# Kernel optimization log

Hardware: AMD Instinct MI355X
Metric: run time of the kernel (lower is better)

The kernel has to match this reference:

```python
import jax, jax.numpy as jnp
import numpy as np

N, L, D, H = 2, 2048, 1024, 16
DK = D // H  # 64


def setup_inputs() -> dict:
    key = jax.random.key(0)
    ks = jax.random.split(key, 8)
    Xq = jax.random.normal(ks[0], (N, L, D), dtype=jnp.float32)
    Xk = jax.random.normal(ks[1], (N, L, D), dtype=jnp.float32)
    Xv = jax.random.normal(ks[2], (N, L, D), dtype=jnp.float32)
    mask_2d = jax.random.randint(ks[3], (N, L, L), 0, 2, dtype=jnp.int32)
    scale = 0.02
    Wq = jax.random.normal(ks[4], (D, D), dtype=jnp.float32) * scale
    Wk = jax.random.normal(ks[5], (D, D), dtype=jnp.float32) * scale
    Wv = jax.random.normal(ks[6], (D, D), dtype=jnp.float32) * scale
    Wo = jax.random.normal(ks[7], (D, D), dtype=jnp.float32) * scale
    return {"Xq": Xq, "Xk": Xk, "Xv": Xv, "Wq": Wq, "Wk": Wk, "Wv": Wv, "Wo": Wo, "mask_2d": mask_2d}


def reference(Xq, Xk, Xv, Wq, Wk, Wv, Wo, mask_2d):
    # Projections (bias=False). Per-head slicing in the original == reshape to [N,L,H,DK].
    Q = (Xq @ Wq).reshape(N, L, H, DK)
    K = (Xk @ Wk).reshape(N, L, H, DK)
    V = (Xv @ Wv).reshape(N, L, H, DK)
    # Scaled dot-product scores: [N, H, L, L]
    scores = jnp.einsum("blhd,bmhd->bhlm", Q, K) / jnp.sqrt(jnp.asarray(DK, scores_dtype(Q)))
    # NOTE: original uses masked_fill(mask==0, 0) BEFORE softmax (zero-fill, not -inf).
    scores = jnp.where(mask_2d[:, None, :, :] == 0, jnp.zeros((), scores.dtype), scores)
    A = jax.nn.softmax(scores, axis=-1)
    O = jnp.einsum("bhlm,bmhd->blhd", A, V).reshape(N, L, D)
    return O @ Wo


def scores_dtype(Q):
    return Q.dtype
```

## Files before the change

kernel.cpp:

```cpp
#include <hip/hip_runtime.h>

#define NB 2
#define L_SEQ 2048
#define NH 16
#define DKH 64
#define DMODEL 1024
#define MROWS (NB * L_SEQ)

typedef __attribute__((ext_vector_type(8))) short short8;
typedef __attribute__((ext_vector_type(4))) float f32x4;

static __device__ __forceinline__ unsigned short f2bf(float f) {
    unsigned u = __float_as_uint(f);
    u += 0x7fffu + ((u >> 16) & 1u);
    return (unsigned short)(u >> 16);
}

static __device__ __forceinline__ float fexp2(float x) {
#if __has_builtin(__builtin_amdgcn_exp2f)
    return __builtin_amdgcn_exp2f(x);
#else
    return __expf(x * 0.6931471806f);
#endif
}

static __device__ __forceinline__ void gll16(const void* g, void* l) {
    __builtin_amdgcn_global_load_lds(
        (const __attribute__((address_space(1))) void*)g,
        (__attribute__((address_space(3))) void*)l, 16, 0, 0);
}

__global__ __launch_bounds__(256)
void cast3(const float* __restrict__ s0, const float* __restrict__ s1,
           const float* __restrict__ s2, unsigned short* __restrict__ dst)
{
    const int z = blockIdx.z;
    const float* src = (z == 0) ? s0 : (z == 1) ? s1 : s2;
    const size_t i4 = (size_t)blockIdx.x * 256 + threadIdx.x;
    float4 v = ((const float4*)src)[i4];
    ushort4 o;
    o.x = f2bf(v.x); o.y = f2bf(v.y); o.z = f2bf(v.z); o.w = f2bf(v.w);
    ((ushort4*)(dst + (size_t)z * 4194304))[i4] = o;
}

__global__ __launch_bounds__(256)
void castWt(const float* __restrict__ w0, const float* __restrict__ w1,
            const float* __restrict__ w2, const float* __restrict__ w3,
            unsigned short* __restrict__ dst)
{
    __shared__ float ts[32][33];
    const int z = blockIdx.z;
    const float* W = (z == 0) ? w0 : (z == 1) ? w1 : (z == 2) ? w2 : w3;
    unsigned short* Wt = dst + (size_t)z * 1048576;

    const int k0 = blockIdx.y * 32;
    const int n0 = blockIdx.x * 32;
    const int t  = threadIdx.x;
    const int r  = t >> 3;
    const int c  = (t & 7) * 4;

    float4 v = *(const float4*)&W[(size_t)(k0 + r) * DMODEL + n0 + c];
    ts[r][c + 0] = v.x; ts[r][c + 1] = v.y; ts[r][c + 2] = v.z; ts[r][c + 3] = v.w;
    __syncthreads();

    ushort4 o;
    o.x = f2bf(ts[c + 0][r]); o.y = f2bf(ts[c + 1][r]);
    o.z = f2bf(ts[c + 2][r]); o.w = f2bf(ts[c + 3][r]);
    *(ushort4*)&Wt[(size_t)(n0 + r) * DMODEL + k0 + c] = o;
}

__global__ __launch_bounds__(256)
void maskbits(const int* __restrict__ mask, unsigned long long* __restrict__ MWT)
{
    const int lane = threadIdx.x & 63;
    const size_t wid = (size_t)blockIdx.x * 4 + (threadIdx.x >> 6);
    const int mv = mask[wid * 64 + lane];
    const unsigned long long bits = __ballot(mv != 0);
    if (lane == 0) {
        const int b   = (int)(wid >> 16);
        const int rem = (int)(wid & 65535);
        const int row = rem >> 5;
        const int wd  = rem & 31;
        MWT[((size_t)b * 32 + wd) * L_SEQ + row] = bits;
    }
}

__global__ __launch_bounds__(256)
void gemm_bf16(const unsigned short* __restrict__ Aall,
               const unsigned short* __restrict__ Ball,
               void* __restrict__ Oall,
               const int out_mode, const size_t a_zs, const size_t b_zs,
               const size_t o_zs)
{
    __shared__ __align__(16) unsigned short As[128 * 32];
    __shared__ __align__(16) unsigned short Bs[128 * 32];
    __shared__ __align__(16) unsigned short Ts[128 * 128];

    const int t    = threadIdx.x;
    const int w    = t >> 6;
    const int lane = t & 63;
    const int z    = blockIdx.z;
    const int m0   = blockIdx.y * 128;
    const int n0   = blockIdx.x * 128;

    const unsigned short* A = Aall + (size_t)z * a_zs;
    const unsigned short* B = Ball + (size_t)z * b_zs;

    const int srow = w * 32 + (lane >> 2);
    const int skc  = (lane & 3) * 8;
    const unsigned short* agp0 = A + (size_t)(m0 + srow) * DMODEL + skc;
    const unsigned short* agp1 = agp0 + (size_t)16 * DMODEL;
    const unsigned short* bgp0 = B + (size_t)(n0 + srow) * DMODEL + skc;
    const unsigned short* bgp1 = bgp0 + (size_t)16 * DMODEL;
    unsigned short* la0 = &As[w * 1024];
    unsigned short* la1 = la0 + 512;
    unsigned short* lb0 = &Bs[w * 1024];
    unsigned short* lb1 = lb0 + 512;

    const int ml = lane & 15;
    const int q  = lane >> 4;
    const int wm = (w >> 1) * 64;
    const int wn = (w & 1) * 64;

    const f32x4 z4 = {0.f, 0.f, 0.f, 0.f};
    f32x4 acc[4][4];
#pragma unroll
    for (int i = 0; i < 4; ++i)
#pragma unroll
        for (int j = 0; j < 4; ++j) acc[i][j] = z4;

    for (int kt = 0; kt < DMODEL; kt += 32) {
        __syncthreads();
        gll16(agp0 + kt, la0);
        gll16(agp1 + kt, la1);
        gll16(bgp0 + kt, lb0);
        gll16(bgp1 + kt, lb1);
        __syncthreads();

        short8 av[4], bv[4];
#pragma unroll
        for (int mt = 0; mt < 4; ++mt)
            av[mt] = *(const short8*)&As[(wm + mt * 16 + ml) * 32 + q * 8];
#pragma unroll
        for (int nt = 0; nt < 4; ++nt)
            bv[nt] = *(const short8*)&Bs[(wn + nt * 16 + ml) * 32 + q * 8];
#pragma unroll
        for (int mt = 0; mt < 4; ++mt)
#pragma unroll
            for (int nt = 0; nt < 4; ++nt)
                acc[mt][nt] = __builtin_amdgcn_mfma_f32_16x16x32_bf16(
                    av[mt], bv[nt], acc[mt][nt], 0, 0, 0);
    }

    if (out_mode == 0) {
        unsigned short* O = (unsigned short*)Oall + (size_t)z * o_zs;
        if (z == 2) {
#pragma unroll
            for (int mt = 0; mt < 4; ++mt) {
                const int trow0 = wm + mt * 16 + q * 4;
                const int ch    = trow0 >> 3;
#pragma unroll
                for (int nt = 0; nt < 4; ++nt) {
                    const int tcol = wn + nt * 16 + ml;
                    const int pc   = (ch & 8) | ((ch & 7) ^ (tcol & 7));
                    ushort4 pv;
                    pv.x = f2bf(acc[mt][nt][0]); pv.y = f2bf(acc[mt][nt][1]);
                    pv.z = f2bf(acc[mt][nt][2]); pv.w = f2bf(acc[mt][nt][3]);
                    *(ushort4*)&Ts[tcol * 128 + pc * 8 + (trow0 & 7)] = pv;
                }
            }
            __syncthreads();
            const int bb = m0 >> 11;
            const int l0 = (m0 & (L_SEQ - 1)) + (t & 15) * 8;
            const int cr = t & 15;
#pragma unroll
            for (int it = 0; it < 8; ++it) {
                const int tcol = (t >> 4) + 16 * it;
                const int pc   = (cr & 8) | ((cr & 7) ^ (tcol & 7));
                short8 vv = *(const short8*)&Ts[tcol * 128 + pc * 8];
                const int n  = n0 + tcol;
                const int hh = n >> 6;
                const int dk = n & (DKH - 1);
                *(short8*)&O[((size_t)(bb * NH + hh) * DKH + dk) * L_SEQ + l0] = vv;
            }
        } else {
#pragma unroll
            for (int mt = 0; mt < 4; ++mt) {
                const int gr0 = m0 + wm + mt * 16 + q * 4;
#pragma unroll
                for (int nt = 0; nt < 4; ++nt) {
                    const int col = n0 + wn + nt * 16 + ml;
                    const int hh  = col >> 6;
                    const int dk  = col & (DKH - 1);
#pragma unroll
                    for (int r = 0; r < 4; ++r) {
                        const int row = gr0 + r;
                        const int bb  = row >> 11;
                        const int l   = row & (L_SEQ - 1);
                        O[(((size_t)(bb * NH + hh) * L_SEQ + l) << 6) + dk] =
                            f2bf(acc[mt][nt][r]);
                    }
                }
            }
        }
    } else {
        float* O = (float*)Oall;
#pragma unroll
        for (int mt = 0; mt < 4; ++mt) {
            const int gr0 = m0 + wm + mt * 16 + q * 4;
#pragma unroll
            for (int nt = 0; nt < 4; ++nt) {
                const int col = n0 + wn + nt * 16 + ml;
#pragma unroll
                for (int r = 0; r < 4; ++r)
                    O[(size_t)(gr0 + r) * DMODEL + col] = acc[mt][nt][r];
            }
        }
    }
}

__global__ __launch_bounds__(256, 4)
void attn_mfma(const unsigned short* __restrict__ Qb,
               const unsigned short* __restrict__ Kb,
               const unsigned short* __restrict__ Vtb,
               const unsigned long long* __restrict__ MWT,
               unsigned short* __restrict__ OB)
{
    __shared__ __align__(16) unsigned short Qs[64 * 64];
    __shared__ __align__(16) unsigned short Ks[64 * 64];
    __shared__ __align__(16) unsigned short Vts[64 * 64];
    __shared__ __align__(16) unsigned short Ps[4][16 * 64];
    __shared__ __align__(16) unsigned long long MskL[64];

    const int t    = threadIdx.x;
    const int w    = t >> 6;
    const int lane = t & 63;
    const int ml   = lane & 15;
    const int quad = lane >> 4;

    const int q0 = blockIdx.x * 64;
    const int h  = blockIdx.y;
    const int b  = blockIdx.z;

    const size_t hoff = (size_t)(b * NH + h) * L_SEQ * DKH;
    const unsigned short* Qh  = Qb  + hoff;
    const unsigned short* Kh  = Kb  + hoff;
    const unsigned short* Vth = Vtb + hoff;

    const int srow = lane >> 3;
    const int sc   = (lane & 7) ^ srow;

    gll16(Qh + (size_t)(q0 + w * 16 + srow) * DKH + sc * 8, &Qs[(w * 16) * 64]);
    gll16(Qh + (size_t)(q0 + w * 16 + 8 + srow) * DKH + sc * 8, &Qs[(w * 16 + 8) * 64]);
    __syncthreads();

    short8 qf[2];
#pragma unroll
    for (int s = 0; s < 2; ++s)
        qf[s] = *(const short8*)
            &Qs[(w * 16 + ml) * 64 + (((s * 4 + quad) ^ (ml & 7)) * 8)];

    const unsigned short* kg0 = Kh + (size_t)(w * 16 + srow) * DKH + sc * 8;
    const unsigned short* kg1 = Kh + (size_t)(w * 16 + 8 + srow) * DKH + sc * 8;
    const unsigned short* vg0 = Vth + (size_t)(w * 16 + srow) * L_SEQ + sc * 8;
    const unsigned short* vg1 = Vth + (size_t)(w * 16 + 8 + srow) * L_SEQ + sc * 8;
    unsigned short* lk0 = &Ks[(w * 16) * 64];
    unsigned short* lk1 = &Ks[(w * 16 + 8) * 64];
    unsigned short* lv0 = &Vts[(w * 16) * 64];
    unsigned short* lv1 = &Vts[(w * 16 + 8) * 64];

    const unsigned long long* mg = MWT + (size_t)b * 32 * L_SEQ + q0 + t;
    unsigned long long m_pf = 0;
    if (t < 64) m_pf = mg[0];

    f32x4 oacc[4];
    const f32x4 z4 = {0.f, 0.f, 0.f, 0.f};
#pragma unroll
    for (int dt = 0; dt < 4; ++dt) oacc[dt] = z4;
    float l_i = 0.f;

    for (int j = 0; j < 32; ++j) {
        __syncthreads();
        gll16(kg0, lk0);  gll16(kg1, lk1);
        gll16(vg0, lv0);  gll16(vg1, lv1);
        kg0 += 64 * DKH;  kg1 += 64 * DKH;
        vg0 += 64;        vg1 += 64;
        if (t < 64) {
            MskL[t] = m_pf;
            if (j < 31) m_pf = mg[(size_t)(j + 1) * L_SEQ];
        }
        __syncthreads();

        f32x4 sacc[4];
#pragma unroll
        for (int kt = 0; kt < 4; ++kt) sacc[kt] = z4;
#pragma unroll
        for (int s = 0; s < 2; ++s) {
            short8 kf[4];
#pragma unroll
            for (int kt = 0; kt < 4; ++kt)
                kf[kt] = *(const short8*)
                    &Ks[(kt * 16 + ml) * 64 + (((s * 4 + quad) ^ (ml & 7)) * 8)];
#pragma unroll
            for (int kt = 0; kt < 4; ++kt)
                sacc[kt] = __builtin_amdgcn_mfma_f32_16x16x32_bf16(
                    kf[kt], qf[s], sacc[kt], 0, 0, 0);
        }

        const unsigned long long wq = MskL[w * 16 + ml] >> (quad * 4);
        float rs = 0.f;
        float p[4][4];
#pragma unroll
        for (int kt = 0; kt < 4; ++kt)
#pragma unroll
            for (int r = 0; r < 4; ++r) {
                const float e = fexp2(sacc[kt][r] * 0.1803368801f);
                const bool bit = (wq >> (kt * 16 + r)) & 1ull;
                p[kt][r] = bit ? e : 1.0f;
                rs += p[kt][r];
            }
        rs += __shfl_xor(rs, 16);
        rs += __shfl_xor(rs, 32);
        l_i += rs;
#pragma unroll
        for (int kt = 0; kt < 4; ++kt) {
            ushort4 pk;
            pk.x = f2bf(p[kt][0]); pk.y = f2bf(p[kt][1]);
            pk.z = f2bf(p[kt][2]); pk.w = f2bf(p[kt][3]);
            const int cp = (kt * 2 + (quad >> 1)) ^ (ml & 7);
            *(ushort4*)&Ps[w][ml * 64 + cp * 8 + (quad & 1) * 4] = pk;
        }

#pragma unroll
        for (int s = 0; s < 2; ++s) {
            const short8 pf = *(const short8*)
                &Ps[w][ml * 64 + (((s * 4 + quad) ^ (ml & 7)) * 8)];
#pragma unroll
            for (int dt = 0; dt < 4; ++dt) {
                const short8 vf = *(const short8*)
                    &Vts[(dt * 16 + ml) * 64 + (((s * 4 + quad) ^ (ml & 7)) * 8)];
                oacc[dt] = __builtin_amdgcn_mfma_f32_16x16x32_bf16(
                    vf, pf, oacc[dt], 0, 0, 0);
            }
        }
    }

    const float inv = 1.0f / l_i;
    const int qrow = q0 + w * 16 + ml;
#pragma unroll
    for (int dt = 0; dt < 4; ++dt)
#pragma unroll
        for (int r = 0; r < 4; ++r) {
            const int d = dt * 16 + quad * 4 + r;
            OB[(size_t)(b * L_SEQ + qrow) * DMODEL + h * DKH + d] =
                f2bf(oacc[dt][r] * inv);
        }
}

extern "C" void kernel_launch(void* const* d_in, const int* in_sizes, int n_in,
                              void* d_out, int out_size, void* d_ws, size_t ws_size,
                              hipStream_t stream)
{
    (void)in_sizes; (void)n_in; (void)out_size; (void)ws_size;

    const float* Xq   = (const float*)d_in[0];
    const float* Xk   = (const float*)d_in[1];
    const float* Xv   = (const float*)d_in[2];
    const float* Wq   = (const float*)d_in[3];
    const float* Wk   = (const float*)d_in[4];
    const float* Wv   = (const float*)d_in[5];
    const float* Wo   = (const float*)d_in[6];
    const int*   mask = (const int*)d_in[7];
    float* out = (float*)d_out;

    char* base = (char*)d_ws;
    unsigned short*     XB  = (unsigned short*)base;
    unsigned short*     WtB = (unsigned short*)(base + (24u << 20));
    unsigned short*     QKV = (unsigned short*)(base + (32u << 20));
    unsigned short*     OB  = (unsigned short*)(base + (56u << 20));
    unsigned long long* MWT = (unsigned long long*)(base + (64u << 20));

    const size_t tsz = (size_t)MROWS * DMODEL;

    cast3<<<dim3(4096, 1, 3), 256, 0, stream>>>(Xq, Xk, Xv, XB);
    castWt<<<dim3(32, 32, 4), 256, 0, stream>>>(Wq, Wk, Wv, Wo, WtB);
    maskbits<<<dim3(32768), 256, 0, stream>>>(mask, MWT);

    gemm_bf16<<<dim3(8, 32, 3), 256, 0, stream>>>(
        XB, WtB, (void*)QKV, 0, tsz, (size_t)DMODEL * DMODEL, tsz);

    attn_mfma<<<dim3(L_SEQ / 64, NH, NB), 256, 0, stream>>>(
        QKV, QKV + tsz, QKV + 2 * tsz, MWT, OB);

    gemm_bf16<<<dim3(8, 32, 1), 256, 0, stream>>>(
        OB, WtB + 3 * (size_t)DMODEL * DMODEL, (void*)out, 1, 0, 0, 0);
}
```

Baseline: 297.9 us.

## Deepen GEMM K-tile with swizzled LDS, fold Q scale, remap attention grid

The GEMM now loads 64-wide K tiles into XOR-swizzled shared memory and reuses that buffer for the transpose staging, which halves the number of barrier pairs and cuts LDS bank conflicts. The softmax scale is folded into the Q projection epilogue, and the mask is applied by multiplying the exponent argument by the bit, which removes a select. The attention launch becomes a 1D grid remapped so that consecutive blocks share K/V heads, aiming for better L2 reuse. Output stores are vectorized and P is packed with a bf16x2 conversion. Folding the scale into bf16 Q adds a small rounding difference.

```diff
diff --git a/kernel.cpp b/kernel.cpp
--- a/kernel.cpp
+++ b/kernel.cpp
@@ -1,4 +1,5 @@
 #include <hip/hip_runtime.h>
+#include <hip/hip_bf16.h>
 
 #define NB 2
 #define L_SEQ 2048
@@ -6,6 +7,7 @@
 #define DKH 64
 #define DMODEL 1024
 #define MROWS (NB * L_SEQ)
+#define QSCALE 0.18033688f
 
 typedef __attribute__((ext_vector_type(8))) short short8;
 typedef __attribute__((ext_vector_type(4))) float f32x4;
@@ -22,6 +24,11 @@
 #else
     return __expf(x * 0.6931471806f);
 #endif
+}
+
+static __device__ __forceinline__ unsigned pk_bf16(float a, float b) {
+    __hip_bfloat162 h = __float22bfloat162_rn(make_float2(a, b));
+    return *reinterpret_cast<unsigned*>(&h);
 }
 
 static __device__ __forceinline__ void gll16(const void* g, void* l) {
@@ -92,9 +99,9 @@
                const int out_mode, const size_t a_zs, const size_t b_zs,
                const size_t o_zs)
 {
-    __shared__ __align__(16) unsigned short As[128 * 32];
-    __shared__ __align__(16) unsigned short Bs[128 * 32];
-    __shared__ __align__(16) unsigned short Ts[128 * 128];
+    __shared__ __align__(16) unsigned short SMEM[16384];
+    unsigned short* As = SMEM;
+    unsigned short* Bs = SMEM + 8192;
 
     const int t    = threadIdx.x;
     const int w    = t >> 6;
@@ -106,16 +113,21 @@
     const unsigned short* A = Aall + (size_t)z * a_zs;
     const unsigned short* B = Ball + (size_t)z * b_zs;
 
-    const int srow = w * 32 + (lane >> 2);
-    const int skc  = (lane & 3) * 8;
-    const unsigned short* agp0 = A + (size_t)(m0 + srow) * DMODEL + skc;
-    const unsigned short* agp1 = agp0 + (size_t)16 * DMODEL;
-    const unsigned short* bgp0 = B + (size_t)(n0 + srow) * DMODEL + skc;
-    const unsigned short* bgp1 = bgp0 + (size_t)16 * DMODEL;
-    unsigned short* la0 = &As[w * 1024];
-    unsigned short* la1 = la0 + 512;
-    unsigned short* lb0 = &Bs[w * 1024];
-    unsigned short* lb1 = lb0 + 512;
+    const int srow = lane >> 3;
+    const int sc   = (lane & 7) ^ srow;
+
+    const unsigned short* ag[4];
+    const unsigned short* bg[4];
+    unsigned short* la[4];
+    unsigned short* lb[4];
+#pragma unroll
+    for (int j = 0; j < 4; ++j) {
+        const int R = w * 32 + j * 8;
+        ag[j] = A + (size_t)(m0 + R + srow) * DMODEL + sc * 8;
+        bg[j] = B + (size_t)(n0 + R + srow) * DMODEL + sc * 8;
+        la[j] = As + R * 64;
+        lb[j] = Bs + R * 64;
+    }
 
     const int ml = lane & 15;
     const int q  = lane >> 4;
@@ -129,32 +141,40 @@
 #pragma unroll
         for (int j = 0; j < 4; ++j) acc[i][j] = z4;
 
-    for (int kt = 0; kt < DMODEL; kt += 32) {
+    for (int kt = 0; kt < DMODEL; kt += 64) {
         __syncthreads();
-        gll16(agp0 + kt, la0);
-        gll16(agp1 + kt, la1);
-        gll16(bgp0 + kt, lb0);
-        gll16(bgp1 + kt, lb1);
+#pragma unroll
+        for (int j = 0; j < 4; ++j) {
+            gll16(ag[j] + kt, la[j]);
+            gll16(bg[j] + kt, lb[j]);
+        }
         __syncthreads();
 
-        short8 av[4], bv[4];
-#pragma unroll
-        for (int mt = 0; mt < 4; ++mt)
-            av[mt] = *(const short8*)&As[(wm + mt * 16 + ml) * 32 + q * 8];
-#pragma unroll
-        for (int nt = 0; nt < 4; ++nt)
-            bv[nt] = *(const short8*)&Bs[(wn + nt * 16 + ml) * 32 + q * 8];
-#pragma unroll
-        for (int mt = 0; mt < 4; ++mt)
+#pragma unroll
+        for (int s = 0; s < 2; ++s) {
+            short8 av[4], bv[4];
+#pragma unroll
+            for (int mt = 0; mt < 4; ++mt)
+                av[mt] = *(const short8*)
+                    &As[(wm + mt * 16 + ml) * 64 + (((s * 4 + q) ^ (ml & 7)) * 8)];
 #pragma unroll
             for (int nt = 0; nt < 4; ++nt)
-                acc[mt][nt] = __builtin_amdgcn_mfma_f32_16x16x32_bf16(
-                    av[mt], bv[nt], acc[mt][nt], 0, 0, 0);
+                bv[nt] = *(const short8*)
+                    &Bs[(wn + nt * 16 + ml) * 64 + (((s * 4 + q) ^ (ml & 7)) * 8)];
+#pragma unroll
+            for (int mt = 0; mt < 4; ++mt)
+#pragma unroll
+                for (int nt = 0; nt < 4; ++nt)
+                    acc[mt][nt] = __builtin_amdgcn_mfma_f32_16x16x32_bf16(
+                        av[mt], bv[nt], acc[mt][nt], 0, 0, 0);
+        }
     }
 
     if (out_mode == 0) {
         unsigned short* O = (unsigned short*)Oall + (size_t)z * o_zs;
         if (z == 2) {
+            __syncthreads();
+            unsigned short* Ts = SMEM;
 #pragma unroll
             for (int mt = 0; mt < 4; ++mt) {
                 const int trow0 = wm + mt * 16 + q * 4;
@@ -184,6 +204,7 @@
                 *(short8*)&O[((size_t)(bb * NH + hh) * DKH + dk) * L_SEQ + l0] = vv;
             }
         } else {
+            const float qs = (z == 0) ? QSCALE : 1.0f;
 #pragma unroll
             for (int mt = 0; mt < 4; ++mt) {
                 const int gr0 = m0 + wm + mt * 16 + q * 4;
@@ -198,7 +219,7 @@
                         const int bb  = row >> 11;
                         const int l   = row & (L_SEQ - 1);
                         O[(((size_t)(bb * NH + hh) * L_SEQ + l) << 6) + dk] =
-                            f2bf(acc[mt][nt][r]);
+                            f2bf(acc[mt][nt][r] * qs);
                     }
                 }
             }
@@ -238,9 +259,12 @@
     const int ml   = lane & 15;
     const int quad = lane >> 4;
 
-    const int q0 = blockIdx.x * 64;
-    const int h  = blockIdx.y;
-    const int b  = blockIdx.z;
+    const int bid = blockIdx.x;
+    const int p   = (bid >> 8) * 8 + (bid & 7);
+    const int jq  = (bid >> 3) & 31;
+    const int h   = p & 15;
+    const int b   = p >> 4;
+    const int q0  = jq * 64;
 
     const size_t hoff = (size_t)(b * NH + h) * L_SEQ * DKH;
     const unsigned short* Qh  = Qb  + hoff;
@@ -308,27 +332,32 @@
         }
 
         const unsigned long long wq = MskL[w * 16 + ml] >> (quad * 4);
+        const unsigned mlo = (unsigned)wq;
+        const unsigned mhi = (unsigned)(wq >> 32);
         float rs = 0.f;
-        float p[4][4];
-#pragma unroll
-        for (int kt = 0; kt < 4; ++kt)
+        float pr[4][4];
+#pragma unroll
+        for (int kt = 0; kt < 4; ++kt) {
+            const unsigned word = (kt < 2) ? mlo : mhi;
+            const int base = (kt & 1) * 16;
 #pragma unroll
             for (int r = 0; r < 4; ++r) {
-                const float e = fexp2(sacc[kt][r] * 0.1803368801f);
-                const bool bit = (wq >> (kt * 16 + r)) & 1ull;
-                p[kt][r] = bit ? e : 1.0f;
-                rs += p[kt][r];
-            }
+                const float mf = (float)((word >> (base + r)) & 1u);
+                const float e  = fexp2(sacc[kt][r] * mf);
+                pr[kt][r] = e;
+                rs += e;
+            }
+        }
         rs += __shfl_xor(rs, 16);
         rs += __shfl_xor(rs, 32);
         l_i += rs;
 #pragma unroll
         for (int kt = 0; kt < 4; ++kt) {
-            ushort4 pk;
-            pk.x = f2bf(p[kt][0]); pk.y = f2bf(p[kt][1]);
-            pk.z = f2bf(p[kt][2]); pk.w = f2bf(p[kt][3]);
+            uint2 pk;
+            pk.x = pk_bf16(pr[kt][0], pr[kt][1]);
+            pk.y = pk_bf16(pr[kt][2], pr[kt][3]);
             const int cp = (kt * 2 + (quad >> 1)) ^ (ml & 7);
-            *(ushort4*)&Ps[w][ml * 64 + cp * 8 + (quad & 1) * 4] = pk;
+            *(uint2*)&Ps[w][ml * 64 + cp * 8 + (quad & 1) * 4] = pk;
         }
 
 #pragma unroll
@@ -348,13 +377,15 @@
     const float inv = 1.0f / l_i;
     const int qrow = q0 + w * 16 + ml;
 #pragma unroll
-    for (int dt = 0; dt < 4; ++dt)
-#pragma unroll
-        for (int r = 0; r < 4; ++r) {
-            const int d = dt * 16 + quad * 4 + r;
-            OB[(size_t)(b * L_SEQ + qrow) * DMODEL + h * DKH + d] =
-                f2bf(oacc[dt][r] * inv);
-        }
+    for (int dt = 0; dt < 4; ++dt) {
+        ushort4 o4;
+        o4.x = f2bf(oacc[dt][0] * inv);
+        o4.y = f2bf(oacc[dt][1] * inv);
+        o4.z = f2bf(oacc[dt][2] * inv);
+        o4.w = f2bf(oacc[dt][3] * inv);
+        *(ushort4*)&OB[(size_t)(b * L_SEQ + qrow) * DMODEL + h * DKH +
+                       dt * 16 + quad * 4] = o4;
+    }
 }
 
 extern "C" void kernel_launch(void* const* d_in, const int* in_sizes, int n_in,
@@ -389,7 +420,7 @@
     gemm_bf16<<<dim3(8, 32, 3), 256, 0, stream>>>(
         XB, WtB, (void*)QKV, 0, tsz, (size_t)DMODEL * DMODEL, tsz);
 
-    attn_mfma<<<dim3(L_SEQ / 64, NH, NB), 256, 0, stream>>>(
+    attn_mfma<<<dim3(1024), 256, 0, stream>>>(
         QKV, QKV + tsz, QKV + 2 * tsz, MWT, OB);
 
     gemm_bf16<<<dim3(8, 32, 1), 256, 0, stream>>>(
```

Result: faster. 271.5 us (-8.9%).
